# Kernel tuning notes

Measured on AMD Instinct MI355X. Metric: run time of the kernel, lower is better.

The kernel has to match this reference:

```python
import jax, jax.numpy as jnp
import numpy as np

TAU = 0.05
BIG_POSITIVE = 1.0e10
COS_EPS = 1e-8  # torch F.cosine_similarity default eps


def setup_inputs() -> dict:
    key = jax.random.key(0)
    k1, k2 = jax.random.split(key)
    b, d = 4096, 1024
    return {
        "batch_feat1": jax.random.normal(k1, (b, d), dtype=jnp.float32),
        "batch_feat2": jax.random.normal(k2, (b, d), dtype=jnp.float32),
        "input_mask": jnp.zeros((b,), dtype=jnp.int32),
    }


def reference(batch_feat1, batch_feat2, input_mask):
    # concat the two views: (2b, d)
    feat = jnp.concatenate([batch_feat1, batch_feat2], axis=0)
    bs = feat.shape[0]
    half = bs // 2

    # cosine similarity = normalize (clamped norm, as in torch) then GEMM
    norm = jnp.maximum(jnp.linalg.norm(feat, axis=-1, keepdims=True), COS_EPS)
    n = feat / norm
    similarity = n @ n.T  # (2b, 2b)

    # mask out self-similarity on the diagonal
    eye = jnp.eye(bs, dtype=similarity.dtype)
    logits = similarity / TAU - eye * BIG_POSITIVE

    idx = jnp.arange(half)
    y_true = jnp.concatenate([idx + half, idx])  # positive pair indices

    # weighted cross entropy: weight[c] = 1 - input_mask[c] (per-class weight)
    weight = (1 - jnp.concatenate([input_mask, input_mask], axis=0)).astype(logits.dtype)
    logp = jax.nn.log_softmax(logits, axis=-1)
    per_example = -jnp.take_along_axis(logp, y_true[:, None], axis=1)[:, 0]
    w = weight[y_true]
    loss = jnp.sum(w * per_example) / jnp.sum(w)
    return (loss, logits, y_true)
```

## Files before the change

kernel.cpp:

```cpp
#include <hip/hip_runtime.h>
#include <math.h>

#define BS 8192
#define HALF 4096
#define DIM 1024
#define BIGP 1.0e10f
#define SQRT_TAU_INV 4.472135955f

typedef __attribute__((ext_vector_type(8))) short bf16x8;
typedef __attribute__((ext_vector_type(4))) float f32x4;

#define GLOAD_LDS16(g, l)                                              \
    __builtin_amdgcn_global_load_lds(                                  \
        (const __attribute__((address_space(1))) void*)(g),            \
        (__attribute__((address_space(3))) void*)(l), 16, 0, 0)

__device__ inline unsigned short f2bf(float f) {
    union { float f; unsigned int u; } c; c.f = f;
    unsigned int u = c.u;
    u += 0x7FFFu + ((u >> 16) & 1u);
    return (unsigned short)(u >> 16);
}

__global__ __launch_bounds__(256) void norm_kernel(const float* __restrict__ f1,
                                                   const float* __restrict__ f2,
                                                   unsigned short* __restrict__ nb) {
    const int row = blockIdx.x;
    const int t = threadIdx.x;
    const float* src = (row < HALF) ? (f1 + (size_t)row * DIM)
                                    : (f2 + (size_t)(row - HALF) * DIM);
    float4 v = reinterpret_cast<const float4*>(src)[t];
    float ss = v.x * v.x + v.y * v.y + v.z * v.z + v.w * v.w;
#pragma unroll
    for (int off = 32; off > 0; off >>= 1) ss += __shfl_down(ss, off, 64);
    __shared__ float red[4];
    if ((t & 63) == 0) red[t >> 6] = ss;
    __syncthreads();
    float tot = red[0] + red[1] + red[2] + red[3];
    float inv = SQRT_TAU_INV / fmaxf(sqrtf(tot), 1e-8f);
    ushort4 o;
    o.x = f2bf(v.x * inv);
    o.y = f2bf(v.y * inv);
    o.z = f2bf(v.z * inv);
    o.w = f2bf(v.w * inv);
    reinterpret_cast<ushort4*>(nb + (size_t)row * DIM)[t] = o;
}

#define BM 128
#define BN 128
#define BK 64

__global__ __launch_bounds__(256) void gemm_kernel(const unsigned short* __restrict__ nb,
                                                   float* __restrict__ logits,
                                                   float* __restrict__ psum,
                                                   float* __restrict__ targ) {
    __shared__ unsigned short As[BM][BK];
    __shared__ unsigned short Bs[BN][BK];
    __shared__ float rowpart[2][BM];
    __shared__ float colpart[2][BM];

    const int t = threadIdx.x;
    const int lane = t & 63;
    const int wid = t >> 6;
    const int wr = wid >> 1;
    const int wc = wid & 1;
    const int lo = lane & 15;
    const int hi = lane >> 4;

    const int id = blockIdx.x;
    int bx = (int)((sqrtf(8.0f * (float)id + 1.0f) - 1.0f) * 0.5f);
    while ((bx + 1) * (bx + 2) / 2 <= id) ++bx;
    while (bx * (bx + 1) / 2 > id) --bx;
    const int by = id - bx * (bx + 1) / 2;
    const bool diag = (bx == by);

    const int rowBase = by * BM;
    const int colBase = bx * BN;

    f32x4 acc[4][4];
#pragma unroll
    for (int m = 0; m < 4; ++m)
#pragma unroll
        for (int n = 0; n < 4; ++n) {
            acc[m][n][0] = 0.f; acc[m][n][1] = 0.f;
            acc[m][n][2] = 0.f; acc[m][n][3] = 0.f;
        }

    const int srow = lane >> 3;
    const int skoff = (((lane & 7) ^ srow) << 3);
    const char* Abase = (const char*)&As[0][0];
    const char* Bbase = (const char*)&Bs[0][0];
    const int rswz = (lo & 7) << 4;

    for (int kt = 0; kt < DIM; kt += BK) {
#pragma unroll
        for (int i = 0; i < 4; ++i) {
            const int chunk = wid * 4 + i;
            const int r = chunk * 8 + srow;
            const unsigned short* gA = nb + (size_t)(rowBase + r) * DIM + kt + skoff;
            GLOAD_LDS16(gA, (char*)&As[0][0] + chunk * 1024);
            const unsigned short* gB = nb + (size_t)(colBase + r) * DIM + kt + skoff;
            GLOAD_LDS16(gB, (char*)&Bs[0][0] + chunk * 1024);
        }
        __syncthreads();

#pragma unroll
        for (int ks = 0; ks < BK; ks += 32) {
            bf16x8 a[4], b[4];
#pragma unroll
            for (int m = 0; m < 4; ++m) {
                const int rr = wr * 64 + m * 16 + lo;
                a[m] = *reinterpret_cast<const bf16x8*>(
                    Abase + rr * 128 + ((ks * 2 + hi * 16) ^ rswz));
            }
#pragma unroll
            for (int n = 0; n < 4; ++n) {
                const int rr = wc * 64 + n * 16 + lo;
                b[n] = *reinterpret_cast<const bf16x8*>(
                    Bbase + rr * 128 + ((ks * 2 + hi * 16) ^ rswz));
            }
#pragma unroll
            for (int m = 0; m < 4; ++m)
#pragma unroll
                for (int n = 0; n < 4; ++n)
                    acc[m][n] = __builtin_amdgcn_mfma_f32_16x16x32_bf16(a[m], b[n], acc[m][n], 0, 0, 0);
        }
        __syncthreads();
    }

    float sums[16];
    float psn[4];
#pragma unroll
    for (int p = 0; p < 16; ++p) sums[p] = 0.f;
#pragma unroll
    for (int n = 0; n < 4; ++n) psn[n] = 0.f;

#pragma unroll
    for (int m = 0; m < 4; ++m) {
#pragma unroll
        for (int n = 0; n < 4; ++n) {
            const int col = colBase + wc * 64 + n * 16 + lo;
#pragma unroll
            for (int r = 0; r < 4; ++r) {
                const int row = rowBase + wr * 64 + m * 16 + hi * 4 + r;
                float v = acc[m][n][r];
                if (row == col) v -= BIGP;
                logits[(size_t)row * BS + col] = v;
                if (col == row + HALF) { targ[row] = v; targ[col] = v; }
                const float e = __expf(v - 20.0f);
                sums[m * 4 + r] += e;
                psn[n] += e;
            }
        }
    }

    if (!diag) {
#pragma unroll
        for (int m = 0; m < 4; ++m) {
            const int trow0 = rowBase + wr * 64 + m * 16 + hi * 4;
#pragma unroll
            for (int n = 0; n < 4; ++n) {
                const int col = colBase + wc * 64 + n * 16 + lo;
                *reinterpret_cast<f32x4*>(&logits[(size_t)col * BS + trow0]) = acc[m][n];
            }
        }
    }

    float sel = 0.f;
#pragma unroll
    for (int p = 0; p < 16; ++p) {
        float s = sums[p];
        s += __shfl_xor(s, 1, 64);
        s += __shfl_xor(s, 2, 64);
        s += __shfl_xor(s, 4, 64);
        s += __shfl_xor(s, 8, 64);
        sel = (lo == p) ? s : sel;
    }
    rowpart[wc][wr * 64 + (lo >> 2) * 16 + hi * 4 + (lo & 3)] = sel;

    if (!diag) {
        float cs0 = psn[0], cs1 = psn[1], cs2 = psn[2], cs3 = psn[3];
        cs0 += __shfl_xor(cs0, 16, 64); cs0 += __shfl_xor(cs0, 32, 64);
        cs1 += __shfl_xor(cs1, 16, 64); cs1 += __shfl_xor(cs1, 32, 64);
        cs2 += __shfl_xor(cs2, 16, 64); cs2 += __shfl_xor(cs2, 32, 64);
        cs3 += __shfl_xor(cs3, 16, 64); cs3 += __shfl_xor(cs3, 32, 64);
        const float cw = (hi == 0) ? cs0 : (hi == 1) ? cs1 : (hi == 2) ? cs2 : cs3;
        colpart[wr][wc * 64 + hi * 16 + lo] = cw;
    }
    __syncthreads();

    if (t < BM) {
        psum[(size_t)bx * BS + rowBase + t] = rowpart[0][t] + rowpart[1][t];
        if (!diag)
            psum[(size_t)by * BS + colBase + t] = colpart[0][t] + colpart[1][t];
    }
}

__global__ __launch_bounds__(256) void reduce_rows_kernel(const float* __restrict__ psum,
                                                          const float* __restrict__ targ,
                                                          const int* __restrict__ mask,
                                                          float* __restrict__ partials,
                                                          float* __restrict__ ytrue_out) {
    const int t = threadIdx.x;
    const int row = blockIdx.x * 256 + t;

    float total = 0.f;
#pragma unroll 8
    for (int cb = 0; cb < 64; ++cb) total += psum[(size_t)cb * BS + row];

    const float pe = -(targ[row] - 20.0f - logf(total));
    const float w = 1.0f - (float)mask[row & (HALF - 1)];
    ytrue_out[row] = (float)((row < HALF) ? row + HALF : row - HALF);

    float a = w * pe, b = w;
#pragma unroll
    for (int off = 32; off > 0; off >>= 1) {
        a += __shfl_down(a, off, 64);
        b += __shfl_down(b, off, 64);
    }
    __shared__ float ra[4], rb[4];
    if ((t & 63) == 0) { ra[t >> 6] = a; rb[t >> 6] = b; }
    __syncthreads();
    if (t == 0) {
        partials[blockIdx.x] = ra[0] + ra[1] + ra[2] + ra[3];
        partials[32 + blockIdx.x] = rb[0] + rb[1] + rb[2] + rb[3];
    }
}

__global__ void loss_kernel(const float* __restrict__ partials,
                            float* __restrict__ loss_out) {
    if (threadIdx.x == 0) {
        float A = 0.f, B = 0.f;
        for (int i = 0; i < 32; ++i) { A += partials[i]; B += partials[32 + i]; }
        loss_out[0] = A / B;
    }
}

extern "C" void kernel_launch(void* const* d_in, const int* in_sizes, int n_in,
                              void* d_out, int out_size, void* d_ws, size_t ws_size,
                              hipStream_t stream) {
    const float* f1 = (const float*)d_in[0];
    const float* f2 = (const float*)d_in[1];
    const int* mask = (const int*)d_in[2];
    float* out = (float*)d_out;

    unsigned short* nb = (unsigned short*)d_ws;
    float* psum = (float*)((char*)d_ws + (size_t)BS * DIM * 2);
    float* targ = psum + (size_t)64 * BS;
    float* partials = targ + BS;
    float* logits = out + 1;
    float* ytrue_out = out + 1 + (size_t)BS * BS;

    norm_kernel<<<BS, 256, 0, stream>>>(f1, f2, nb);

    const int ntri = (BS / BM) * (BS / BM + 1) / 2;
    gemm_kernel<<<ntri, 256, 0, stream>>>(nb, logits, psum, targ);

    reduce_rows_kernel<<<BS / 256, 256, 0, stream>>>(psum, targ, mask, partials, ytrue_out);
    loss_kernel<<<1, 64, 0, stream>>>(partials, out);
}
```

Baseline: 170.9 us.

## Transpose accumulators in registers for vectorized row logits stores; drop LDS reduction

The epilogue now uses lane shuffles to transpose each 4x4 MFMA output fragment, so the direct (row-major) logits store becomes a 16-byte vector store instead of scalar strided stores. Row and column exp-sums are written straight to a doubled psum buffer (128 partial slots per row), which removes the shared-memory staging arrays and the final __syncthreads. Launch bounds now request 5 blocks per CU. In exchange there are extra shuffles, and the row-reduce kernel reads twice as many partials.

```diff
diff --git a/kernel.cpp b/kernel.cpp
--- a/kernel.cpp
+++ b/kernel.cpp
@@ -50,14 +50,12 @@
 #define BN 128
 #define BK 64
 
-__global__ __launch_bounds__(256) void gemm_kernel(const unsigned short* __restrict__ nb,
-                                                   float* __restrict__ logits,
-                                                   float* __restrict__ psum,
-                                                   float* __restrict__ targ) {
+__global__ __launch_bounds__(256, 5) void gemm_kernel(const unsigned short* __restrict__ nb,
+                                                      float* __restrict__ logits,
+                                                      float* __restrict__ psum,
+                                                      float* __restrict__ targ) {
     __shared__ unsigned short As[BM][BK];
     __shared__ unsigned short Bs[BN][BK];
-    __shared__ float rowpart[2][BM];
-    __shared__ float colpart[2][BM];
 
     const int t = threadIdx.x;
     const int lane = t & 63;
@@ -128,31 +126,83 @@
         __syncthreads();
     }
 
-    float sums[16];
-    float psn[4];
-#pragma unroll
-    for (int p = 0; p < 16; ++p) sums[p] = 0.f;
-#pragma unroll
-    for (int n = 0; n < 4; ++n) psn[n] = 0.f;
-
+    if (diag) {
+#pragma unroll
+        for (int m = 0; m < 4; ++m) {
+            const int lr0 = wr * 64 + m * 16 + hi * 4;
+#pragma unroll
+            for (int n = 0; n < 4; ++n) {
+                const int lc = wc * 64 + n * 16 + lo;
+#pragma unroll
+                for (int r = 0; r < 4; ++r)
+                    if (lr0 + r == lc) acc[m][n][r] -= BIGP;
+            }
+        }
+    }
+
+    float psn[4] = {0.f, 0.f, 0.f, 0.f};
+#pragma unroll
+    for (int m = 0; m < 4; ++m)
+#pragma unroll
+        for (int n = 0; n < 4; ++n)
+#pragma unroll
+            for (int r = 0; r < 4; ++r)
+                psn[n] += __expf(acc[m][n][r] - 20.0f);
+#pragma unroll
+    for (int n = 0; n < 4; ++n) {
+        psn[n] += __shfl_xor(psn[n], 16, 64);
+        psn[n] += __shfl_xor(psn[n], 32, 64);
+    }
+    if (!diag) {
+        const float cw = (hi == 0) ? psn[0] : (hi == 1) ? psn[1]
+                       : (hi == 2) ? psn[2] : psn[3];
+        psum[(size_t)(2 * by + wr) * BS + colBase + wc * 64 + hi * 16 + lo] = cw;
+    }
+
+    const int p = lane & 3;
+    const int g = (lane >> 2) & 3;
+    float rsum[4] = {0.f, 0.f, 0.f, 0.f};
 #pragma unroll
     for (int m = 0; m < 4; ++m) {
+        const int row = rowBase + wr * 64 + m * 16 + hi * 4 + p;
 #pragma unroll
         for (int n = 0; n < 4; ++n) {
-            const int col = colBase + wc * 64 + n * 16 + lo;
-#pragma unroll
-            for (int r = 0; r < 4; ++r) {
-                const int row = rowBase + wr * 64 + m * 16 + hi * 4 + r;
-                float v = acc[m][n][r];
-                if (row == col) v -= BIGP;
-                logits[(size_t)row * BS + col] = v;
-                if (col == row + HALF) { targ[row] = v; targ[col] = v; }
-                const float e = __expf(v - 20.0f);
-                sums[m * 4 + r] += e;
-                psn[n] += e;
-            }
-        }
-    }
+            const float t0 = acc[m][n][0], t1 = acc[m][n][1];
+            const float t2 = acc[m][n][2], t3 = acc[m][n][3];
+            const float s0 = __shfl_xor(t1, 1, 64);
+            const float s1 = __shfl_xor(t0, 1, 64);
+            const float s2 = __shfl_xor(t3, 1, 64);
+            const float s3 = __shfl_xor(t2, 1, 64);
+            const float a0 = (p & 1) ? s0 : t0;
+            const float a1 = (p & 1) ? t1 : s1;
+            const float a2 = (p & 1) ? s2 : t2;
+            const float a3 = (p & 1) ? t3 : s3;
+            const float u0 = __shfl_xor(a2, 2, 64);
+            const float u1 = __shfl_xor(a3, 2, 64);
+            const float u2 = __shfl_xor(a0, 2, 64);
+            const float u3 = __shfl_xor(a1, 2, 64);
+            f32x4 w;
+            w[0] = (p & 2) ? u0 : a0;
+            w[1] = (p & 2) ? u1 : a1;
+            w[2] = (p & 2) ? a2 : u2;
+            w[3] = (p & 2) ? a3 : u3;
+            const int cb0 = colBase + wc * 64 + n * 16 + 4 * g;
+            *reinterpret_cast<f32x4*>(&logits[(size_t)row * BS + cb0]) = w;
+#pragma unroll
+            for (int q = 0; q < 4; ++q) {
+                rsum[m] += __expf(w[q] - 20.0f);
+                if (cb0 + q == row + HALF) { targ[row] = w[q]; targ[row + HALF] = w[q]; }
+            }
+        }
+    }
+#pragma unroll
+    for (int m = 0; m < 4; ++m) {
+        rsum[m] += __shfl_xor(rsum[m], 4, 64);
+        rsum[m] += __shfl_xor(rsum[m], 8, 64);
+    }
+    const float rw = (g == 0) ? rsum[0] : (g == 1) ? rsum[1]
+                   : (g == 2) ? rsum[2] : rsum[3];
+    psum[(size_t)(2 * bx + wc) * BS + rowBase + wr * 64 + g * 16 + hi * 4 + p] = rw;
 
     if (!diag) {
 #pragma unroll
@@ -164,35 +214,6 @@
                 *reinterpret_cast<f32x4*>(&logits[(size_t)col * BS + trow0]) = acc[m][n];
             }
         }
-    }
-
-    float sel = 0.f;
-#pragma unroll
-    for (int p = 0; p < 16; ++p) {
-        float s = sums[p];
-        s += __shfl_xor(s, 1, 64);
-        s += __shfl_xor(s, 2, 64);
-        s += __shfl_xor(s, 4, 64);
-        s += __shfl_xor(s, 8, 64);
-        sel = (lo == p) ? s : sel;
-    }
-    rowpart[wc][wr * 64 + (lo >> 2) * 16 + hi * 4 + (lo & 3)] = sel;
-
-    if (!diag) {
-        float cs0 = psn[0], cs1 = psn[1], cs2 = psn[2], cs3 = psn[3];
-        cs0 += __shfl_xor(cs0, 16, 64); cs0 += __shfl_xor(cs0, 32, 64);
-        cs1 += __shfl_xor(cs1, 16, 64); cs1 += __shfl_xor(cs1, 32, 64);
-        cs2 += __shfl_xor(cs2, 16, 64); cs2 += __shfl_xor(cs2, 32, 64);
-        cs3 += __shfl_xor(cs3, 16, 64); cs3 += __shfl_xor(cs3, 32, 64);
-        const float cw = (hi == 0) ? cs0 : (hi == 1) ? cs1 : (hi == 2) ? cs2 : cs3;
-        colpart[wr][wc * 64 + hi * 16 + lo] = cw;
-    }
-    __syncthreads();
-
-    if (t < BM) {
-        psum[(size_t)bx * BS + rowBase + t] = rowpart[0][t] + rowpart[1][t];
-        if (!diag)
-            psum[(size_t)by * BS + colBase + t] = colpart[0][t] + colpart[1][t];
     }
 }
 
@@ -206,7 +227,7 @@
 
     float total = 0.f;
 #pragma unroll 8
-    for (int cb = 0; cb < 64; ++cb) total += psum[(size_t)cb * BS + row];
+    for (int cb = 0; cb < 128; ++cb) total += psum[(size_t)cb * BS + row];
 
     const float pe = -(targ[row] - 20.0f - logf(total));
     const float w = 1.0f - (float)mask[row & (HALF - 1)];
@@ -246,7 +267,7 @@
 
     unsigned short* nb = (unsigned short*)d_ws;
     float* psum = (float*)((char*)d_ws + (size_t)BS * DIM * 2);
-    float* targ = psum + (size_t)64 * BS;
+    float* targ = psum + (size_t)128 * BS;
     float* partials = targ + BS;
     float* logits = out + 1;
     float* ytrue_out = out + 1 + (size_t)BS * BS;
```

Measured after the change: 457.6 us. 2.68x slower.
